# Kernel tuning notes

Hardware: AMD Instinct MI355X
Metric: run time of the kernel (lower is better)

The kernel has to match this reference:

```python
import jax, jax.numpy as jnp
import numpy as np

B, T, K = 256, 512, 128


def setup_inputs() -> dict:
    key = jax.random.key(0)
    k1, k2, k3, k4 = jax.random.split(key, 4)
    emissions = jax.random.normal(k1, (B, T, K), jnp.float32)
    tag_ids = jax.random.randint(k2, (B, T), 0, K, dtype=jnp.int32)
    lengths = jnp.maximum(jax.random.randint(k3, (B,), 0, T + 1, dtype=jnp.int32), 1)
    # learned CRF transition matrix (transition_weight * learning_rate_multiplier)
    transitions = jax.random.normal(k4, (K, K), jnp.float32) * 0.1
    return {"emissions": emissions, "tag_ids": tag_ids, "lengths": lengths,
            "transitions": transitions}


def _log_norm(emissions, transitions, lengths):
    # forward algorithm (log-sum-exp semiring scan over time)
    t = emissions.shape[1]
    alpha0 = emissions[:, 0]  # [B,K]
    valid = jnp.arange(1, t)[:, None] < lengths[None, :]  # [T-1,B]

    def step(alpha, inp):
        emit_t, v = inp  # [B,K], [B]
        new = jax.nn.logsumexp(alpha[:, :, None] + transitions[None], axis=1) + emit_t
        return jnp.where(v[:, None], new, alpha), None

    alpha, _ = jax.lax.scan(step, alpha0, (jnp.swapaxes(emissions[:, 1:], 0, 1), valid))
    return jax.nn.logsumexp(alpha, axis=-1)  # [B]


def _sequence_score(emissions, transitions, tag_ids, lengths):
    t = emissions.shape[1]
    mask = (jnp.arange(t)[None, :] < lengths[:, None]).astype(emissions.dtype)  # [B,T]
    unary = jnp.take_along_axis(emissions, tag_ids[..., None], axis=-1)[..., 0]  # [B,T]
    unary_score = jnp.sum(unary * mask, axis=1)
    pair = transitions[tag_ids[:, :-1], tag_ids[:, 1:]]  # [B,T-1]
    binary_score = jnp.sum(pair * mask[:, 1:], axis=1)  # prefix mask: t+1 valid => t valid
    return unary_score + binary_score


def _viterbi_decode(emissions, transitions, lengths):
    t = emissions.shape[1]
    k = emissions.shape[2]
    v0 = emissions[:, 0]  # [B,K]
    valid = jnp.arange(1, t)[:, None] < lengths[None, :]  # [T-1,B]
    identity_bp = jnp.arange(k, dtype=jnp.int32)[None, :]  # pass-through for padding

    def fwd(v, inp):
        emit_t, va = inp
        scores = v[:, :, None] + transitions[None]  # [B,K,K]
        bp = jnp.argmax(scores, axis=1).astype(jnp.int32)  # [B,K]
        new = jnp.max(scores, axis=1) + emit_t
        v_new = jnp.where(va[:, None], new, v)
        bp = jnp.where(va[:, None], bp, identity_bp)
        return v_new, bp

    v_final, bps = jax.lax.scan(fwd, v0, (jnp.swapaxes(emissions[:, 1:], 0, 1), valid))
    last_tag = jnp.argmax(v_final, axis=-1).astype(jnp.int32)  # [B]

    def back(tag, bp_t):
        prev = jnp.take_along_axis(bp_t, tag[:, None], axis=1)[:, 0]
        return prev, tag  # emit tag_{t+1}, carry tag_t

    first_tag, tags_rest = jax.lax.scan(back, last_tag, bps, reverse=True)
    decoded = jnp.concatenate([first_tag[None], tags_rest], axis=0)  # [T,B]
    return jnp.swapaxes(decoded, 0, 1)  # [B,T]


def reference(emissions, tag_ids, lengths, transitions):
    log_likelihood = _sequence_score(emissions, transitions, tag_ids, lengths) \
        - _log_norm(emissions, transitions, lengths)
    loss = -jnp.mean(log_likelihood)
    decoded = _viterbi_decode(emissions, transitions, lengths)
    mask = (jnp.arange(emissions.shape[1])[None, :] < lengths[:, None]).astype(jnp.int32)
    is_equal = (tag_ids == decoded).astype(jnp.int32)
    tag_accuracy = jnp.sum(is_equal * mask) / jnp.sum(mask)
    return loss, decoded, tag_accuracy
```

## Files before the change

kernel.cpp:

```cpp
#include <hip/hip_runtime.h>

#define T_ 512
#define K_ 128
#define B_ 256


__global__ __launch_bounds__(256, 2) void crf_main(
    const float* __restrict__ emissions,
    const int* __restrict__ tag_ids,
    const int* __restrict__ lengths,
    const float* __restrict__ transitions,
    float* __restrict__ out,
    float* __restrict__ ws_ll,
    int* __restrict__ ws_cnt)
{
    const int bid = blockIdx.x;
    const int tid = threadIdx.x;

    if (bid < B_) {
        __shared__ __align__(16) float eaBuf[2][K_];
        __shared__ __align__(16) float wmax[4];
        __shared__ float redLDS[4];

        const int b   = bid;
        const int len = lengths[b];
        const float* emB = emissions + (size_t)b * T_ * K_;
        const int*  tagB = tag_ids + b * T_;

        {
            float s = 0.f;
            #pragma unroll
            for (int h = 0; h < 2; ++h) {
                int t = tid + h * 256;
                if (t < len) {
                    int tg = tagB[t];
                    float v = emB[t * K_ + tg];
                    if (t >= 1) v += transitions[tagB[t - 1] * K_ + tg];
                    s += v;
                }
            }
            #pragma unroll
            for (int m = 1; m < 64; m <<= 1) s += __shfl_xor(s, m);
            if ((tid & 63) == 0) redLDS[tid >> 6] = s;
        }

        const int j = tid >> 1;
        const int c = tid & 1;

        float tbl[64];
        #pragma unroll
        for (int k = 0; k < 64; ++k)
            tbl[k] = __expf(transitions[(c * 64 + k) * K_ + j]);

        {
            float e0 = emB[j];
            if (c == 0) eaBuf[0][j] = __expf(e0);
            float wm = e0;
            #pragma unroll
            for (int m = 1; m < 64; m <<= 1) wm = fmaxf(wm, __shfl_xor(wm, m));
            if ((tid & 63) == 0) wmax[tid >> 6] = wm;
        }
        __syncthreads();

        int cur = 0;
        float Sr = 0.f;
        float emN = emB[K_ + j];

        for (int t = 1; t < len; ++t) {
            float emC = emN;
            int tn = (t + 1 < T_) ? (t + 1) : t;
            emN = emB[tn * K_ + j];

            float Sw;
            if (((t - 1) & 3) == 0) {
                float4 wv = *(const float4*)&wmax[0];
                Sw = fmaxf(fmaxf(wv.x, wv.y), fmaxf(wv.z, wv.w));
            } else Sw = Sr;

            const float* ea = &eaBuf[cur][c * 64];
            float a0 = 0.f, a1 = 0.f, a2 = 0.f, a3 = 0.f;
            #pragma unroll
            for (int k = 0; k < 16; ++k) {
                float4 e4 = *(const float4*)(ea + 4 * k);
                a0 = fmaf(e4.x, tbl[4 * k + 0], a0);
                a1 = fmaf(e4.y, tbl[4 * k + 1], a1);
                a2 = fmaf(e4.z, tbl[4 * k + 2], a2);
                a3 = fmaf(e4.w, tbl[4 * k + 3], a3);
            }
            float dot = (a0 + a1) + (a2 + a3);
            dot += __shfl_xor(dot, 1);

            float an = __logf(dot) + Sr + emC;
            if (c == 0) eaBuf[cur ^ 1][j] = __expf(an - Sw);
            Sr = Sw;

            if (((t - 1) & 3) == 3) {
                float wm = an;
                #pragma unroll
                for (int m = 1; m < 64; m <<= 1) wm = fmaxf(wm, __shfl_xor(wm, m));
                if ((tid & 63) == 0) wmax[tid >> 6] = wm;
            }
            cur ^= 1;
            __syncthreads();
        }

        float logZv = 0.f;
        if (tid < 64) {
            float s = eaBuf[cur][tid] + eaBuf[cur][tid + 64];
            #pragma unroll
            for (int m = 1; m < 64; m <<= 1) s += __shfl_xor(s, m);
            logZv = Sr + __logf(s);
        }
        if (tid == 0) {
            float sc = redLDS[0] + redLDS[1] + redLDS[2] + redLDS[3];
            ws_ll[b] = sc - logZv;
        }

    } else {
        __shared__ unsigned char bpLDS[T_ * K_];
        __shared__ __align__(16) float vaBuf[2][K_];
        __shared__ unsigned char decLDS[T_];
        __shared__ int redILDS[4];
        __shared__ int ltagLDS;

        const int b   = bid - B_;
        const int len = lengths[b];
        const float* emB = emissions + (size_t)b * T_ * K_;
        const int*  tagB = tag_ids + b * T_;

        const int j = tid >> 1;
        const int c = tid & 1;

        float tbl[64];
        #pragma unroll
        for (int k = 0; k < 64; ++k)
            tbl[k] = transitions[(c * 64 + k) * K_ + j];

        {
            float e0 = emB[j];
            if (c == 0) vaBuf[0][j] = e0;
        }
        __syncthreads();

        int cur = 0;
        float emN = emB[K_ + j];

        for (int t = 1; t < len; ++t) {
            float emC = emN;
            int tn = (t + 1 < T_) ? (t + 1) : t;
            emN = emB[tn * K_ + j];

            const float* va = &vaBuf[cur][c * 64];
            float mB = -3.4028235e38f;
            int arg = 0;
            #pragma unroll
            for (int k = 0; k < 16; ++k) {
                float4 v4 = *(const float4*)(va + 4 * k);
                float s0 = v4.x + tbl[4 * k + 0]; if (s0 > mB) { mB = s0; arg = 4 * k + 0; }
                float s1 = v4.y + tbl[4 * k + 1]; if (s1 > mB) { mB = s1; arg = 4 * k + 1; }
                float s2 = v4.z + tbl[4 * k + 2]; if (s2 > mB) { mB = s2; arg = 4 * k + 2; }
                float s3 = v4.w + tbl[4 * k + 3]; if (s3 > mB) { mB = s3; arg = 4 * k + 3; }
            }
            arg += c * 64;
            float om = __shfl_xor(mB, 1);
            int   oa = __shfl_xor(arg, 1);
            float mLow  = c ? om : mB;   int aLow  = c ? oa : arg;
            float mHigh = c ? mB : om;   int aHigh = c ? arg : oa;
            float mF; int aF;
            if (mHigh > mLow) { mF = mHigh; aF = aHigh; } else { mF = mLow; aF = aLow; }
            if (c == 0) {
                vaBuf[cur ^ 1][j] = mF + emC;
                bpLDS[t * K_ + j] = (unsigned char)aF;
            }
            cur ^= 1;
            __syncthreads();
        }

        if (tid < 64) {
            int l = tid;
            float m = vaBuf[cur][l]; int a = l;
            float v2 = vaBuf[cur][l + 64];
            if (v2 > m) { m = v2; a = l + 64; }
            #pragma unroll
            for (int sft = 1; sft < 64; sft <<= 1) {
                float om = __shfl_xor(m, sft);
                int   oa = __shfl_xor(a, sft);
                if (om > m || (om == m && oa < a)) { m = om; a = oa; }
            }
            if (l == 0) ltagLDS = a;
        }
        __syncthreads();

        if (tid == 0) {
            int tg = ltagLDS;
            for (int t = T_ - 1; t >= 1; --t) {
                decLDS[t] = (unsigned char)tg;
                if (t < len) tg = bpLDS[t * K_ + tg];
            }
            decLDS[0] = (unsigned char)tg;
        }
        __syncthreads();

        {
            int good = 0;
            #pragma unroll
            for (int h = 0; h < 2; ++h) {
                int t = tid + h * 256;
                int dv = decLDS[t];
                out[1 + b * T_ + t] = (float)dv;
                good += (t < len && tagB[t] == dv) ? 1 : 0;
            }
            #pragma unroll
            for (int m = 1; m < 64; m <<= 1) good += __shfl_xor(good, m);
            if ((tid & 63) == 0) redILDS[tid >> 6] = good;
        }
        __syncthreads();

        if (tid == 0)
            ws_cnt[b] = redILDS[0] + redILDS[1] + redILDS[2] + redILDS[3];
    }
}

__global__ void crf_final(const float* __restrict__ ws_ll,
                          const int* __restrict__ ws_cnt,
                          const int* __restrict__ lengths,
                          float* __restrict__ out)
{
    __shared__ float sll[4];
    __shared__ int scnt[4], slen[4];
    int tid = threadIdx.x;
    float ll = ws_ll[tid];
    int   cn = ws_cnt[tid];
    int   L  = lengths[tid];
    #pragma unroll
    for (int m = 1; m < 64; m <<= 1) {
        ll += __shfl_xor(ll, m);
        cn += __shfl_xor(cn, m);
        L  += __shfl_xor(L, m);
    }
    if ((tid & 63) == 0) { sll[tid >> 6] = ll; scnt[tid >> 6] = cn; slen[tid >> 6] = L; }
    __syncthreads();
    if (tid == 0) {
        float llS = sll[0] + sll[1] + sll[2] + sll[3];
        int   cS  = scnt[0] + scnt[1] + scnt[2] + scnt[3];
        int   LS  = slen[0] + slen[1] + slen[2] + slen[3];
        out[0] = -llS / (float)B_;
        out[1 + B_ * T_] = (float)cS / (float)LS;
    }
}

extern "C" void kernel_launch(void* const* d_in, const int* in_sizes, int n_in,
                              void* d_out, int out_size, void* d_ws, size_t ws_size,
                              hipStream_t stream) {
    const float* emissions   = (const float*)d_in[0];
    const int*   tag_ids     = (const int*)d_in[1];
    const int*   lengths     = (const int*)d_in[2];
    const float* transitions = (const float*)d_in[3];
    float* out = (float*)d_out;

    float* ws_ll  = (float*)d_ws;
    int*   ws_cnt = (int*)((char*)d_ws + B_ * sizeof(float));

    crf_main<<<2 * B_, 256, 0, stream>>>(emissions, tag_ids, lengths, transitions,
                                         out, ws_ll, ws_cnt);
    crf_final<<<1, B_, 0, stream>>>(ws_ll, ws_cnt, lengths, out);
}
```

Baseline: 614.1 us.

## Remap threads to compute two output tags over quarter-K slices with skewed LDS

Each group of four threads now owns two adjacent output tags and each thread covers a 32-entry slice of the source tags, so every float4 LDS read of the alpha/Viterbi vector feeds two FMAs or compares instead of one. The shared alpha buffers use a padded (36-float stride) skewed layout to avoid bank conflicts, and the Viterbi argmax becomes a tree reduction with a two-step cross-lane shuffle. Emissions and transitions are loaded as float2 and backpointers are stored as 16-bit pairs. In exchange the per-thread reduction is deeper, each step needs more shuffles, and register pressure rises.

```diff
diff --git a/kernel.cpp b/kernel.cpp
--- a/kernel.cpp
+++ b/kernel.cpp
@@ -3,6 +3,7 @@
 #define T_ 512
 #define K_ 128
 #define B_ 256
+#define SKW(i) ((((i) >> 5) * 36) + ((i) & 31))
 
 
 __global__ __launch_bounds__(256, 2) void crf_main(
@@ -17,8 +18,13 @@
     const int bid = blockIdx.x;
     const int tid = threadIdx.x;
 
+    const int g  = tid >> 2;
+    const int rg = tid & 3;
+    const int j0 = 2 * g;
+    const int wiA = (g >> 4) * 36 + 2 * (g & 15);
+
     if (bid < B_) {
-        __shared__ __align__(16) float eaBuf[2][K_];
+        __shared__ __align__(16) float eaBuf[2][4 * 36];
         __shared__ __align__(16) float wmax[4];
         __shared__ float redLDS[4];
 
@@ -44,18 +50,21 @@
             if ((tid & 63) == 0) redLDS[tid >> 6] = s;
         }
 
-        const int j = tid >> 1;
-        const int c = tid & 1;
-
         float tbl[64];
         #pragma unroll
-        for (int k = 0; k < 64; ++k)
-            tbl[k] = __expf(transitions[(c * 64 + k) * K_ + j]);
+        for (int k = 0; k < 32; ++k) {
+            float2 tr = *(const float2*)&transitions[(rg * 32 + k) * K_ + j0];
+            tbl[2 * k + 0] = __expf(tr.x);
+            tbl[2 * k + 1] = __expf(tr.y);
+        }
 
         {
-            float e0 = emB[j];
-            if (c == 0) eaBuf[0][j] = __expf(e0);
-            float wm = e0;
+            float2 e0 = *(const float2*)(emB + j0);
+            if (rg == 0) {
+                float2 w2; w2.x = __expf(e0.x); w2.y = __expf(e0.y);
+                *(float2*)&eaBuf[0][wiA] = w2;
+            }
+            float wm = fmaxf(e0.x, e0.y);
             #pragma unroll
             for (int m = 1; m < 64; m <<= 1) wm = fmaxf(wm, __shfl_xor(wm, m));
             if ((tid & 63) == 0) wmax[tid >> 6] = wm;
@@ -64,12 +73,12 @@
 
         int cur = 0;
         float Sr = 0.f;
-        float emN = emB[K_ + j];
+        float2 emN = *(const float2*)(emB + K_ + j0);
 
         for (int t = 1; t < len; ++t) {
-            float emC = emN;
+            float2 emC = emN;
             int tn = (t + 1 < T_) ? (t + 1) : t;
-            emN = emB[tn * K_ + j];
+            emN = *(const float2*)(emB + tn * K_ + j0);
 
             float Sw;
             if (((t - 1) & 3) == 0) {
@@ -77,25 +86,36 @@
                 Sw = fmaxf(fmaxf(wv.x, wv.y), fmaxf(wv.z, wv.w));
             } else Sw = Sr;
 
-            const float* ea = &eaBuf[cur][c * 64];
-            float a0 = 0.f, a1 = 0.f, a2 = 0.f, a3 = 0.f;
-            #pragma unroll
-            for (int k = 0; k < 16; ++k) {
-                float4 e4 = *(const float4*)(ea + 4 * k);
-                a0 = fmaf(e4.x, tbl[4 * k + 0], a0);
-                a1 = fmaf(e4.y, tbl[4 * k + 1], a1);
-                a2 = fmaf(e4.z, tbl[4 * k + 2], a2);
-                a3 = fmaf(e4.w, tbl[4 * k + 3], a3);
-            }
-            float dot = (a0 + a1) + (a2 + a3);
-            dot += __shfl_xor(dot, 1);
-
-            float an = __logf(dot) + Sr + emC;
-            if (c == 0) eaBuf[cur ^ 1][j] = __expf(an - Sw);
+            const float* ea = &eaBuf[cur][rg * 36];
+            float a00 = 0.f, a01 = 0.f, a02 = 0.f, a03 = 0.f;
+            float a10 = 0.f, a11 = 0.f, a12 = 0.f, a13 = 0.f;
+            #pragma unroll
+            for (int m = 0; m < 8; ++m) {
+                float4 e4 = *(const float4*)(ea + 4 * m);
+                a00 = fmaf(e4.x, tbl[8 * m + 0], a00);
+                a10 = fmaf(e4.x, tbl[8 * m + 1], a10);
+                a01 = fmaf(e4.y, tbl[8 * m + 2], a01);
+                a11 = fmaf(e4.y, tbl[8 * m + 3], a11);
+                a02 = fmaf(e4.z, tbl[8 * m + 4], a02);
+                a12 = fmaf(e4.z, tbl[8 * m + 5], a12);
+                a03 = fmaf(e4.w, tbl[8 * m + 6], a03);
+                a13 = fmaf(e4.w, tbl[8 * m + 7], a13);
+            }
+            float d0 = (a00 + a01) + (a02 + a03);
+            float d1 = (a10 + a11) + (a12 + a13);
+            d0 += __shfl_xor(d0, 1); d0 += __shfl_xor(d0, 2);
+            d1 += __shfl_xor(d1, 1); d1 += __shfl_xor(d1, 2);
+
+            float an0 = __logf(d0) + Sr + emC.x;
+            float an1 = __logf(d1) + Sr + emC.y;
+            if (rg == 0) {
+                float2 w2; w2.x = __expf(an0 - Sw); w2.y = __expf(an1 - Sw);
+                *(float2*)&eaBuf[cur ^ 1][wiA] = w2;
+            }
             Sr = Sw;
 
             if (((t - 1) & 3) == 3) {
-                float wm = an;
+                float wm = fmaxf(an0, an1);
                 #pragma unroll
                 for (int m = 1; m < 64; m <<= 1) wm = fmaxf(wm, __shfl_xor(wm, m));
                 if ((tid & 63) == 0) wmax[tid >> 6] = wm;
@@ -106,7 +126,7 @@
 
         float logZv = 0.f;
         if (tid < 64) {
-            float s = eaBuf[cur][tid] + eaBuf[cur][tid + 64];
+            float s = eaBuf[cur][SKW(tid)] + eaBuf[cur][SKW(tid + 64)];
             #pragma unroll
             for (int m = 1; m < 64; m <<= 1) s += __shfl_xor(s, m);
             logZv = Sr + __logf(s);
@@ -118,7 +138,7 @@
 
     } else {
         __shared__ unsigned char bpLDS[T_ * K_];
-        __shared__ __align__(16) float vaBuf[2][K_];
+        __shared__ __align__(16) float vaBuf[2][4 * 36];
         __shared__ unsigned char decLDS[T_];
         __shared__ int redILDS[4];
         __shared__ int ltagLDS;
@@ -128,49 +148,76 @@
         const float* emB = emissions + (size_t)b * T_ * K_;
         const int*  tagB = tag_ids + b * T_;
 
-        const int j = tid >> 1;
-        const int c = tid & 1;
-
         float tbl[64];
         #pragma unroll
-        for (int k = 0; k < 64; ++k)
-            tbl[k] = transitions[(c * 64 + k) * K_ + j];
+        for (int k = 0; k < 32; ++k) {
+            float2 tr = *(const float2*)&transitions[(rg * 32 + k) * K_ + j0];
+            tbl[2 * k + 0] = tr.x;
+            tbl[2 * k + 1] = tr.y;
+        }
 
         {
-            float e0 = emB[j];
-            if (c == 0) vaBuf[0][j] = e0;
+            float2 e0 = *(const float2*)(emB + j0);
+            if (rg == 0) *(float2*)&vaBuf[0][wiA] = e0;
         }
         __syncthreads();
 
         int cur = 0;
-        float emN = emB[K_ + j];
+        float2 emN = *(const float2*)(emB + K_ + j0);
 
         for (int t = 1; t < len; ++t) {
-            float emC = emN;
+            float2 emC = emN;
             int tn = (t + 1 < T_) ? (t + 1) : t;
-            emN = emB[tn * K_ + j];
-
-            const float* va = &vaBuf[cur][c * 64];
-            float mB = -3.4028235e38f;
-            int arg = 0;
-            #pragma unroll
-            for (int k = 0; k < 16; ++k) {
-                float4 v4 = *(const float4*)(va + 4 * k);
-                float s0 = v4.x + tbl[4 * k + 0]; if (s0 > mB) { mB = s0; arg = 4 * k + 0; }
-                float s1 = v4.y + tbl[4 * k + 1]; if (s1 > mB) { mB = s1; arg = 4 * k + 1; }
-                float s2 = v4.z + tbl[4 * k + 2]; if (s2 > mB) { mB = s2; arg = 4 * k + 2; }
-                float s3 = v4.w + tbl[4 * k + 3]; if (s3 > mB) { mB = s3; arg = 4 * k + 3; }
-            }
-            arg += c * 64;
-            float om = __shfl_xor(mB, 1);
-            int   oa = __shfl_xor(arg, 1);
-            float mLow  = c ? om : mB;   int aLow  = c ? oa : arg;
-            float mHigh = c ? mB : om;   int aHigh = c ? arg : oa;
-            float mF; int aF;
-            if (mHigh > mLow) { mF = mHigh; aF = aHigh; } else { mF = mLow; aF = aLow; }
-            if (c == 0) {
-                vaBuf[cur ^ 1][j] = mF + emC;
-                bpLDS[t * K_ + j] = (unsigned char)aF;
+            emN = *(const float2*)(emB + tn * K_ + j0);
+
+            const float* va = &vaBuf[cur][rg * 36];
+            float v0[8], v1[8];
+            int   g0[8], g1[8];
+            #pragma unroll
+            for (int m = 0; m < 8; ++m) {
+                float4 e4 = *(const float4*)(va + 4 * m);
+                float s0 = e4.x + tbl[8 * m + 0];
+                float s1 = e4.y + tbl[8 * m + 2];
+                float s2 = e4.z + tbl[8 * m + 4];
+                float s3 = e4.w + tbl[8 * m + 6];
+                float mA; int aA;
+                if (s1 > s0) { mA = s1; aA = 4 * m + 1; } else { mA = s0; aA = 4 * m + 0; }
+                float mC; int aC;
+                if (s3 > s2) { mC = s3; aC = 4 * m + 3; } else { mC = s2; aC = 4 * m + 2; }
+                if (mC > mA) { v0[m] = mC; g0[m] = aC; } else { v0[m] = mA; g0[m] = aA; }
+                float u0 = e4.x + tbl[8 * m + 1];
+                float u1 = e4.y + tbl[8 * m + 3];
+                float u2 = e4.z + tbl[8 * m + 5];
+                float u3 = e4.w + tbl[8 * m + 7];
+                float nA; int bA;
+                if (u1 > u0) { nA = u1; bA = 4 * m + 1; } else { nA = u0; bA = 4 * m + 0; }
+                float nC; int bC;
+                if (u3 > u2) { nC = u3; bC = 4 * m + 3; } else { nC = u2; bC = 4 * m + 2; }
+                if (nC > nA) { v1[m] = nC; g1[m] = bC; } else { v1[m] = nA; g1[m] = bA; }
+            }
+            #pragma unroll
+            for (int st = 1; st < 8; st <<= 1) {
+                #pragma unroll
+                for (int k = 0; k < 8; k += 2 * st) {
+                    if (v0[k + st] > v0[k]) { v0[k] = v0[k + st]; g0[k] = g0[k + st]; }
+                    if (v1[k + st] > v1[k]) { v1[k] = v1[k + st]; g1[k] = g1[k + st]; }
+                }
+            }
+            float m0 = v0[0];  int a0i = g0[0] + rg * 32;
+            float m1 = v1[0];  int a1i = g1[0] + rg * 32;
+
+            #pragma unroll
+            for (int sft = 1; sft <= 2; sft <<= 1) {
+                float o0 = __shfl_xor(m0, sft); int b0 = __shfl_xor(a0i, sft);
+                if (o0 > m0 || (o0 == m0 && b0 < a0i)) { m0 = o0; a0i = b0; }
+                float o1 = __shfl_xor(m1, sft); int b1 = __shfl_xor(a1i, sft);
+                if (o1 > m1 || (o1 == m1 && b1 < a1i)) { m1 = o1; a1i = b1; }
+            }
+            if (rg == 0) {
+                float2 nv; nv.x = m0 + emC.x; nv.y = m1 + emC.y;
+                *(float2*)&vaBuf[cur ^ 1][wiA] = nv;
+                *(unsigned short*)&bpLDS[t * K_ + j0] =
+                    (unsigned short)((a0i & 0xff) | ((a1i & 0xff) << 8));
             }
             cur ^= 1;
             __syncthreads();
@@ -178,8 +225,8 @@
 
         if (tid < 64) {
             int l = tid;
-            float m = vaBuf[cur][l]; int a = l;
-            float v2 = vaBuf[cur][l + 64];
+            float m = vaBuf[cur][SKW(l)]; int a = l;
+            float v2 = vaBuf[cur][SKW(l + 64)];
             if (v2 > m) { m = v2; a = l + 64; }
             #pragma unroll
             for (int sft = 1; sft < 64; sft <<= 1) {
```

New measurement: 720.5 us. 17.3% more time.
